# Kernel optimization log

Measured on AMD Instinct MI355X. Metric: run time of the kernel, lower is better.

The kernel has to match this reference:

```python
import jax, jax.numpy as jnp
import numpy as np

V, E, H, N, T, L = 32000, 1024, 1024, 64, 32, 196


def setup_inputs() -> dict:
    key = jax.random.key(0)
    ks = jax.random.split(key, 12)
    s = 0.02
    return {
        "inputs": jax.random.randint(ks[0], (N, T), 0, V, dtype=jnp.int32),
        "img_features": jax.random.normal(ks[1], (N, L, H), dtype=jnp.float32),
        "emb": jax.random.normal(ks[2], (V, E), dtype=jnp.float32) * s,
        "w_ih1": jax.random.normal(ks[3], (4 * H, E), dtype=jnp.float32) * s,
        "w_hh1": jax.random.normal(ks[4], (4 * H, H), dtype=jnp.float32) * s,
        "b_ih1": jax.random.normal(ks[5], (4 * H,), dtype=jnp.float32) * s,
        "b_hh1": jax.random.normal(ks[6], (4 * H,), dtype=jnp.float32) * s,
        "w_ih2": jax.random.normal(ks[7], (4 * H, 2 * H), dtype=jnp.float32) * s,
        "w_hh2": jax.random.normal(ks[8], (4 * H, H), dtype=jnp.float32) * s,
        "b_ih2": jax.random.normal(ks[9], (4 * H,), dtype=jnp.float32) * s,
        "b_hh2": jax.random.normal(ks[10], (4 * H,), dtype=jnp.float32) * s,
    }


def _lstm_cell(x, h, c, w_ih, w_hh, b_ih, b_hh):
    # PyTorch LSTMCell: gates ordered i, f, g, o
    g = x @ w_ih.T + b_ih + h @ w_hh.T + b_hh
    i, f, gg, o = jnp.split(g, 4, axis=-1)
    c_new = jax.nn.sigmoid(f) * c + jax.nn.sigmoid(i) * jnp.tanh(gg)
    h_new = jax.nn.sigmoid(o) * jnp.tanh(c_new)
    return h_new, c_new


def reference(inputs, img_features, emb, w_ih1, w_hh1, b_ih1, b_hh1,
              w_ih2, w_hh2, b_ih2, b_hh2):
    n, t = inputs.shape
    hdim = w_hh1.shape[1]
    embedded = emb[inputs]                      # (N, T, E)
    # faithful to original: .view(T, N, -1) is a reshape, NOT a transpose
    xs = embedded.reshape(t, n, -1)             # (T, N, E)

    def step(carry, x_t):
        h1, c1, h2, c2 = carry
        h1, c1 = _lstm_cell(x_t, h1, c1, w_ih1, w_hh1, b_ih1, b_hh1)
        # attention: raw dot-product weights (no softmax in original)
        alpha = jnp.einsum('nd,nld->nl', h1, img_features)   # (N, L)
        v_att = jnp.einsum('nl,nld->nd', alpha, img_features) # (N, D)
        x2 = jnp.concatenate([v_att, h1], axis=1)             # (N, 2H)
        h2, c2 = _lstm_cell(x2, h2, c2, w_ih2, w_hh2, b_ih2, b_hh2)
        return (h1, c1, h2, c2), h2

    zeros = jnp.zeros((n, hdim), dtype=img_features.dtype)
    init = (zeros, zeros, zeros, zeros)
    _, hs = jax.lax.scan(step, init, xs)        # (T, N, H)
    # faithful to original: cat along dim 0 then .view(N, T, -1) == reshape
    return hs.reshape(n, t, -1)
```

## Files before the change

kernel.cpp:

```cpp
#include <hip/hip_runtime.h>
#include <math.h>

typedef __attribute__((ext_vector_type(8))) short bf16x8;
typedef __attribute__((ext_vector_type(4))) short short4v;
typedef __attribute__((ext_vector_type(4))) float f32x4;

__device__ __forceinline__ float sigm(float x) { return 1.f / (1.f + expf(-x)); }

__device__ __forceinline__ float bf2f(short x) {
    unsigned u = ((unsigned)(unsigned short)x) << 16;
    float f; __builtin_memcpy(&f, &u, 4); return f;
}
__device__ __forceinline__ short f2bf(float f) {
    unsigned u; __builtin_memcpy(&u, &f, 4);
    unsigned r = (u + 0x7fffu + ((u >> 16) & 1u)) >> 16;
    return (short)r;
}

#define OFF_C1      0u
#define OFF_C2      262144u
#define OFF_H2A     524288u
#define OFF_H2B     655360u
#define OFF_H1HI    786432u
#define OFF_H1LO    5111808u
#define OFF_H1F     9437184u
#define OFF_X0HI    17825792u
#define OFF_X0LO    22020096u
#define OFF_B1      26214400u
#define OFF_B2      26230784u
#define OFF_WHH1HI  26247168u
#define OFF_WHH1LO  34635776u
#define OFF_WIH1HI  43024384u
#define OFF_WIH1LO  51412992u
#define OFF_WHH2HI  59801600u
#define OFF_WVHI    68190208u
#define OFF_WVLO    76578816u
#define OFF_WH2HI   84967424u
#define OFF_X12     93356032u

__global__ __launch_bounds__(256) void zero_ws(float4* __restrict__ p) {
    int i = blockIdx.x * 256 + threadIdx.x;
    p[i] = make_float4(0.f, 0.f, 0.f, 0.f);
}

__global__ __launch_bounds__(256) void perm_w_split(const float* __restrict__ src,
                                                    short* __restrict__ hi,
                                                    short* __restrict__ lo,
                                                    int rs, int co) {
    int idx = blockIdx.x * 256 + threadIdx.x;
    int jp = idx >> 8;
    int kq = idx & 255;
    int jsrc = (jp & 3) * 1024 + (jp >> 2);
    float4 v = *(const float4*)(src + (size_t)jsrc * rs + co + kq * 4);
    float a[4] = {v.x, v.y, v.z, v.w};
    short4v h, l;
    #pragma unroll
    for (int e = 0; e < 4; e++) {
        short q = f2bf(a[e]);
        h[e] = q;
        l[e] = f2bf(a[e] - bf2f(q));
    }
    *(short4v*)(hi + (size_t)jp * 1024 + kq * 4) = h;
    *(short4v*)(lo + (size_t)jp * 1024 + kq * 4) = l;
}

__global__ __launch_bounds__(256) void bias_prep(
    const float* __restrict__ bi1, const float* __restrict__ bh1,
    const float* __restrict__ bi2, const float* __restrict__ bh2,
    float* __restrict__ b1p, float* __restrict__ b2p) {
    int jp = blockIdx.x * 256 + threadIdx.x;
    int j = (jp & 3) * 1024 + (jp >> 2);
    b1p[jp] = bi1[j] + bh1[j];
    b2p[jp] = bi2[j] + bh2[j];
}

__global__ __launch_bounds__(256) void gather_x0_split(
    const int* __restrict__ tokens, const float* __restrict__ emb,
    short* __restrict__ hi, short* __restrict__ lo) {
    int idx = blockIdx.x * 256 + threadIdx.x;
    int p = idx >> 8;
    int k0 = (idx & 255) * 4;
    int tok = tokens[p];
    float4 v = *(const float4*)(emb + (size_t)tok * 1024 + k0);
    float a[4] = {v.x, v.y, v.z, v.w};
    short4v h, l;
    #pragma unroll
    for (int e = 0; e < 4; e++) {
        short q = f2bf(a[e]);
        h[e] = q;
        l[e] = f2bf(a[e] - bf2f(q));
    }
    *(short4v*)(hi + (size_t)p * 1024 + k0) = h;
    *(short4v*)(lo + (size_t)p * 1024 + k0) = l;
}

__global__ __launch_bounds__(256) void big_gemm(
    const short* __restrict__ A0, const short* __restrict__ A1s,
    const short* __restrict__ A2s, const short* __restrict__ A3s,
    const short* __restrict__ B0, const short* __restrict__ B1s,
    const short* __restrict__ B2s, const short* __restrict__ B3s,
    const float* __restrict__ bias, float* __restrict__ C, int K) {
    __shared__ short As[128 * 40];
    __shared__ short Bs[128 * 40];
    int tid = threadIdx.x;
    int n0 = blockIdx.x * 128;
    int m0 = blockIdx.y * 128;
    int lane = tid & 63, w = tid >> 6;
    int wm = (w >> 1) * 64, wn = (w & 1) * 64;
    int quad = lane >> 4, l16 = lane & 15;
    int srow = tid >> 2;
    int skc = (tid & 3) * 8;

    f32x4 acc[4][4];
    f32x4 z4 = {0.f, 0.f, 0.f, 0.f};
    #pragma unroll
    for (int i = 0; i < 4; i++)
        #pragma unroll
        for (int j = 0; j < 4; j++) acc[i][j] = z4;

    for (int k0 = 0; k0 < K; k0 += 32) {
        int seg = k0 >> 10;
        const short* Ab = (seg == 0) ? A0 : (seg == 1) ? A1s : (seg == 2) ? A2s : A3s;
        const short* Bb = (seg == 0) ? B0 : (seg == 1) ? B1s : (seg == 2) ? B2s : B3s;
        int kk = (k0 & 1023) + skc;
        const short* ga = Ab + (size_t)(m0 + srow) * 1024 + kk;
        const short* gb = Bb + (size_t)(n0 + srow) * 1024 + kk;
        bf16x8 av0 = *(const bf16x8*)ga;
        bf16x8 av1 = *(const bf16x8*)(ga + 64 * 1024);
        bf16x8 bv0 = *(const bf16x8*)gb;
        bf16x8 bv1 = *(const bf16x8*)(gb + 64 * 1024);
        __syncthreads();
        *(bf16x8*)&As[srow * 40 + skc] = av0;
        *(bf16x8*)&As[(srow + 64) * 40 + skc] = av1;
        *(bf16x8*)&Bs[srow * 40 + skc] = bv0;
        *(bf16x8*)&Bs[(srow + 64) * 40 + skc] = bv1;
        __syncthreads();
        bf16x8 af[4], bfr[4];
        #pragma unroll
        for (int im = 0; im < 4; im++)
            af[im] = *(const bf16x8*)&As[(wm + im * 16 + l16) * 40 + quad * 8];
        #pragma unroll
        for (int in = 0; in < 4; in++)
            bfr[in] = *(const bf16x8*)&Bs[(wn + in * 16 + l16) * 40 + quad * 8];
        #pragma unroll
        for (int im = 0; im < 4; im++)
            #pragma unroll
            for (int in = 0; in < 4; in++)
                acc[im][in] = __builtin_amdgcn_mfma_f32_16x16x32_bf16(
                    af[im], bfr[in], acc[im][in], 0, 0, 0);
    }
    #pragma unroll
    for (int in = 0; in < 4; in++) {
        int j = n0 + wn + in * 16 + l16;
        float bsv = bias[j];
        #pragma unroll
        for (int im = 0; im < 4; im++) {
            #pragma unroll
            for (int r = 0; r < 4; r++) {
                int p = m0 + wm + im * 16 + quad * 4 + r;
                C[(size_t)p * 4096 + j] = acc[im][in][r] + bsv;
            }
        }
    }
}

__global__ __launch_bounds__(256) void cell_step1(
    const short* __restrict__ Ahi, const short* __restrict__ Alo,
    const short* __restrict__ Whi, const short* __restrict__ Wlo,
    const float* __restrict__ Xg, float* __restrict__ c,
    short* __restrict__ hhi_o, short* __restrict__ hlo_o,
    float* __restrict__ hf_o) {
    __shared__ float red[4 * 64 * 16];
    int tid = threadIdx.x;
    int lane = tid & 63, w = tid >> 6;
    int quad = lane >> 4, l16 = lane & 15;
    int g = blockIdx.x;
    int kbase = w * 256;

    f32x4 acc[4];
    f32x4 z4 = {0.f, 0.f, 0.f, 0.f};
    acc[0] = z4; acc[1] = z4; acc[2] = z4; acc[3] = z4;

    const short* bh = Whi + (size_t)(g * 16 + l16) * 1024 + kbase + quad * 8;
    const short* bl = Wlo + (size_t)(g * 16 + l16) * 1024 + kbase + quad * 8;
    const short* ah = Ahi + (size_t)l16 * 1024 + kbase + quad * 8;
    const short* al = Alo + (size_t)l16 * 1024 + kbase + quad * 8;
    #pragma unroll
    for (int i = 0; i < 8; i++) {
        int k = i * 32;
        bf16x8 Bh = *(const bf16x8*)(bh + k);
        bf16x8 Bl = *(const bf16x8*)(bl + k);
        #pragma unroll
        for (int mt = 0; mt < 4; mt++) {
            bf16x8 Ah = *(const bf16x8*)(ah + mt * 16 * 1024 + k);
            bf16x8 Al = *(const bf16x8*)(al + mt * 16 * 1024 + k);
            acc[mt] = __builtin_amdgcn_mfma_f32_16x16x32_bf16(Ah, Bh, acc[mt], 0, 0, 0);
            acc[mt] = __builtin_amdgcn_mfma_f32_16x16x32_bf16(Al, Bh, acc[mt], 0, 0, 0);
            acc[mt] = __builtin_amdgcn_mfma_f32_16x16x32_bf16(Ah, Bl, acc[mt], 0, 0, 0);
        }
    }
    #pragma unroll
    for (int mt = 0; mt < 4; mt++)
        #pragma unroll
        for (int r = 0; r < 4; r++) {
            int s = mt * 16 + quad * 4 + r;
            red[(w * 64 + s) * 16 + l16] = acc[mt][r];
        }
    __syncthreads();

    int s = tid >> 2, dl = tid & 3;
    float gi = 0.f, gf = 0.f, gg = 0.f, go = 0.f;
    #pragma unroll
    for (int w2 = 0; w2 < 4; w2++) {
        const float* rp = &red[(w2 * 64 + s) * 16 + dl * 4];
        gi += rp[0]; gf += rp[1]; gg += rp[2]; go += rp[3];
    }
    float4 xg = *(const float4*)(Xg + (size_t)s * 4096 + g * 16 + dl * 4);
    gi += xg.x; gf += xg.y; gg += xg.z; go += xg.w;
    int d = g * 4 + dl;
    float cold = c[s * 1024 + d];
    float cn = sigm(gf) * cold + sigm(gi) * tanhf(gg);
    c[s * 1024 + d] = cn;
    float hn = sigm(go) * tanhf(cn);
    short q = f2bf(hn);
    hhi_o[s * 1024 + d] = q;
    hlo_o[s * 1024 + d] = f2bf(hn - bf2f(q));
    hf_o[s * 1024 + d] = hn;
}

__global__ __launch_bounds__(256) void cell_step2(
    const short* __restrict__ Aprev, const short* __restrict__ W,
    const float* __restrict__ Xg, float* __restrict__ c,
    short* __restrict__ hout_bf, float* __restrict__ hout_f32) {
    __shared__ float red[4 * 64 * 16];
    int tid = threadIdx.x;
    int lane = tid & 63, w = tid >> 6;
    int quad = lane >> 4, l16 = lane & 15;
    int g = blockIdx.x;
    int kbase = w * 256;

    f32x4 acc[4];
    f32x4 z4 = {0.f, 0.f, 0.f, 0.f};
    acc[0] = z4; acc[1] = z4; acc[2] = z4; acc[3] = z4;

    const short* brow = W + (size_t)(g * 16 + l16) * 1024 + kbase + quad * 8;
    const short* arow = Aprev + (size_t)l16 * 1024 + kbase + quad * 8;
    #pragma unroll
    for (int i = 0; i < 8; i++) {
        int k = i * 32;
        bf16x8 b = *(const bf16x8*)(brow + k);
        #pragma unroll
        for (int mt = 0; mt < 4; mt++) {
            bf16x8 a = *(const bf16x8*)(arow + mt * 16 * 1024 + k);
            acc[mt] = __builtin_amdgcn_mfma_f32_16x16x32_bf16(a, b, acc[mt], 0, 0, 0);
        }
    }
    #pragma unroll
    for (int mt = 0; mt < 4; mt++)
        #pragma unroll
        for (int r = 0; r < 4; r++) {
            int s = mt * 16 + quad * 4 + r;
            red[(w * 64 + s) * 16 + l16] = acc[mt][r];
        }
    __syncthreads();

    int s = tid >> 2, dl = tid & 3;
    float gi = 0.f, gf = 0.f, gg = 0.f, go = 0.f;
    #pragma unroll
    for (int w2 = 0; w2 < 4; w2++) {
        const float* rp = &red[(w2 * 64 + s) * 16 + dl * 4];
        gi += rp[0]; gf += rp[1]; gg += rp[2]; go += rp[3];
    }
    float4 xg = *(const float4*)(Xg + (size_t)s * 4096 + g * 16 + dl * 4);
    gi += xg.x; gf += xg.y; gg += xg.z; go += xg.w;
    int d = g * 4 + dl;
    float cold = c[s * 1024 + d];
    float cn = sigm(gf) * cold + sigm(gi) * tanhf(gg);
    c[s * 1024 + d] = cn;
    float hn = sigm(go) * tanhf(cn);
    hout_bf[s * 1024 + d] = f2bf(hn);
    hout_f32[s * 1024 + d] = hn;
}

__global__ __launch_bounds__(256) void attn_batch(
    const float* __restrict__ H1f, const float* __restrict__ F,
    short* __restrict__ Vhi, short* __restrict__ Vlo) {
    __shared__ float vs[4][4][1024];
    int n = blockIdx.x, tg = blockIdx.y;
    int tid = threadIdx.x, lane = tid & 63, w = tid >> 6;

    float h[4][16];
    #pragma unroll
    for (int tt = 0; tt < 4; tt++) {
        const float* hp = H1f + ((size_t)((tg * 4 + tt) * 64 + n)) * 1024 + lane * 16;
        #pragma unroll
        for (int j = 0; j < 4; j++) {
            float4 v = *(const float4*)(hp + j * 4);
            h[tt][j * 4 + 0] = v.x; h[tt][j * 4 + 1] = v.y;
            h[tt][j * 4 + 2] = v.z; h[tt][j * 4 + 3] = v.w;
        }
    }
    float vacc[4][16];
    #pragma unroll
    for (int tt = 0; tt < 4; tt++)
        #pragma unroll
        for (int j = 0; j < 16; j++) vacc[tt][j] = 0.f;

    const float* Fn = F + ((size_t)n * 196) * 1024 + lane * 16;
    for (int l = w; l < 196; l += 4) {
        const float* fr = Fn + (size_t)l * 1024;
        float f[16];
        #pragma unroll
        for (int j = 0; j < 4; j++) {
            float4 v = *(const float4*)(fr + j * 4);
            f[j * 4 + 0] = v.x; f[j * 4 + 1] = v.y;
            f[j * 4 + 2] = v.z; f[j * 4 + 3] = v.w;
        }
        float p[4] = {0.f, 0.f, 0.f, 0.f};
        #pragma unroll
        for (int tt = 0; tt < 4; tt++)
            #pragma unroll
            for (int j = 0; j < 16; j++) p[tt] += f[j] * h[tt][j];
        #pragma unroll
        for (int off = 32; off > 0; off >>= 1) {
            #pragma unroll
            for (int tt = 0; tt < 4; tt++) p[tt] += __shfl_xor(p[tt], off, 64);
        }
        #pragma unroll
        for (int tt = 0; tt < 4; tt++)
            #pragma unroll
            for (int j = 0; j < 16; j++) vacc[tt][j] += p[tt] * f[j];
    }
    #pragma unroll
    for (int tt = 0; tt < 4; tt++)
        #pragma unroll
        for (int j4 = 0; j4 < 4; j4++) {
            float4 v;
            v.x = vacc[tt][j4 * 4 + 0]; v.y = vacc[tt][j4 * 4 + 1];
            v.z = vacc[tt][j4 * 4 + 2]; v.w = vacc[tt][j4 * 4 + 3];
            *(float4*)&vs[w][tt][lane * 16 + j4 * 4] = v;
        }
    __syncthreads();
    int d0 = tid * 4;
    #pragma unroll
    for (int tt = 0; tt < 4; tt++) {
        float4 a = *(const float4*)&vs[0][tt][d0];
        float4 b = *(const float4*)&vs[1][tt][d0];
        float4 cc = *(const float4*)&vs[2][tt][d0];
        float4 e = *(const float4*)&vs[3][tt][d0];
        float sv[4];
        sv[0] = a.x + b.x + cc.x + e.x;
        sv[1] = a.y + b.y + cc.y + e.y;
        sv[2] = a.z + b.z + cc.z + e.z;
        sv[3] = a.w + b.w + cc.w + e.w;
        short4v b1, b2;
        #pragma unroll
        for (int e2 = 0; e2 < 4; e2++) {
            short q = f2bf(sv[e2]);
            b1[e2] = q;
            b2[e2] = f2bf(sv[e2] - bf2f(q));
        }
        size_t row = ((size_t)(tg * 4 + tt) * 64 + n) * 1024 + d0;
        *(short4v*)(Vhi + row) = b1;
        *(short4v*)(Vlo + row) = b2;
    }
}

extern "C" void kernel_launch(void* const* d_in, const int* in_sizes, int n_in,
                              void* d_out, int out_size, void* d_ws, size_t ws_size,
                              hipStream_t stream) {
    const int*   tokens = (const int*)d_in[0];
    const float* imgf   = (const float*)d_in[1];
    const float* emb    = (const float*)d_in[2];
    const float* w_ih1  = (const float*)d_in[3];
    const float* w_hh1  = (const float*)d_in[4];
    const float* b_ih1  = (const float*)d_in[5];
    const float* b_hh1  = (const float*)d_in[6];
    const float* w_ih2  = (const float*)d_in[7];
    const float* w_hh2  = (const float*)d_in[8];
    const float* b_ih2  = (const float*)d_in[9];
    const float* b_hh2  = (const float*)d_in[10];
    float* out = (float*)d_out;
    char* ws = (char*)d_ws;

    float* c1     = (float*)(ws + OFF_C1);
    float* c2     = (float*)(ws + OFF_C2);
    short* h2a    = (short*)(ws + OFF_H2A);
    short* h2b    = (short*)(ws + OFF_H2B);
    short* H1hi   = (short*)(ws + OFF_H1HI);
    short* H1lo   = (short*)(ws + OFF_H1LO);
    float* H1f    = (float*)(ws + OFF_H1F);
    short* X0hi   = (short*)(ws + OFF_X0HI);
    short* X0lo   = (short*)(ws + OFF_X0LO);
    short* Vhi    = (short*)(ws + OFF_X0HI);
    short* Vlo    = (short*)(ws + OFF_X0LO);
    float* bias1p = (float*)(ws + OFF_B1);
    float* bias2p = (float*)(ws + OFF_B2);
    short* whh1hi = (short*)(ws + OFF_WHH1HI);
    short* whh1lo = (short*)(ws + OFF_WHH1LO);
    short* wih1hi = (short*)(ws + OFF_WIH1HI);
    short* wih1lo = (short*)(ws + OFF_WIH1LO);
    short* whh2hi = (short*)(ws + OFF_WHH2HI);
    short* wvhi   = (short*)(ws + OFF_WVHI);
    short* wvlo   = (short*)(ws + OFF_WVLO);
    short* wh2hi  = (short*)(ws + OFF_WH2HI);
    float* X12    = (float*)(ws + OFF_X12);
    short* dump   = (short*)(ws + OFF_X12);

    zero_ws<<<192, 256, 0, stream>>>((float4*)(ws + OFF_C1));
    zero_ws<<<32, 256, 0, stream>>>((float4*)(ws + OFF_H1HI));
    zero_ws<<<32, 256, 0, stream>>>((float4*)(ws + OFF_H1LO));
    perm_w_split<<<4096, 256, 0, stream>>>(w_hh1, whh1hi, whh1lo, 1024, 0);
    perm_w_split<<<4096, 256, 0, stream>>>(w_ih1, wih1hi, wih1lo, 1024, 0);
    perm_w_split<<<4096, 256, 0, stream>>>(w_hh2, whh2hi, dump, 1024, 0);
    perm_w_split<<<4096, 256, 0, stream>>>(w_ih2, wvhi, wvlo, 2048, 0);
    perm_w_split<<<4096, 256, 0, stream>>>(w_ih2, wh2hi, dump, 2048, 1024);
    bias_prep<<<16, 256, 0, stream>>>(b_ih1, b_hh1, b_ih2, b_hh2, bias1p, bias2p);
    gather_x0_split<<<2048, 256, 0, stream>>>(tokens, emb, X0hi, X0lo);

    big_gemm<<<dim3(32, 16), 256, 0, stream>>>(
        X0hi, X0lo, X0hi, X0hi,
        wih1hi, wih1hi, wih1lo, wih1hi,
        bias1p, X12, 3072);

    for (int t = 0; t < 32; t++) {
        cell_step1<<<256, 256, 0, stream>>>(
            H1hi + (size_t)t * 65536, H1lo + (size_t)t * 65536,
            whh1hi, whh1lo, X12 + (size_t)t * 262144, c1,
            H1hi + (size_t)(t + 1) * 65536, H1lo + (size_t)(t + 1) * 65536,
            H1f + (size_t)t * 65536);
    }

    attn_batch<<<dim3(64, 8), 256, 0, stream>>>(H1f, imgf, Vhi, Vlo);

    big_gemm<<<dim3(32, 16), 256, 0, stream>>>(
        Vhi, Vlo, Vhi, H1hi + 65536,
        wvhi, wvhi, wvlo, wh2hi,
        bias2p, X12, 4096);

    for (int t = 0; t < 32; t++) {
        short* h2p = (t & 1) ? h2b : h2a;
        short* h2c = (t & 1) ? h2a : h2b;
        cell_step2<<<256, 256, 0, stream>>>(
            h2p, whh2hi, X12 + (size_t)t * 262144, c2,
            h2c, out + (size_t)t * 65536);
    }
}
```

Baseline: 1.189 ms.

## Replace per-timestep LSTM cell launches with persistent cooperative kernels using grid sync

The two recurrent loops, each 32 separate kernel launches, become one cooperative persistent kernel per layer. Each block holds its slice of the recurrent weights in registers for all timesteps and keeps the cell state in a register instead of global memory. Timesteps are separated by grid.sync(). This removes launch overhead, repeated weight reloads and the c-state round trips, at the cost of grid-barrier latency and higher register pressure.

```diff
diff --git a/kernel.cpp b/kernel.cpp
--- a/kernel.cpp
+++ b/kernel.cpp
@@ -1,5 +1,8 @@
 #include <hip/hip_runtime.h>
+#include <hip/hip_cooperative_groups.h>
 #include <math.h>
+
+namespace cg = cooperative_groups;
 
 typedef __attribute__((ext_vector_type(8))) short bf16x8;
 typedef __attribute__((ext_vector_type(4))) short short4v;
@@ -20,7 +23,6 @@
 #define OFF_C1      0u
 #define OFF_C2      262144u
 #define OFF_H2A     524288u
-#define OFF_H2B     655360u
 #define OFF_H1HI    786432u
 #define OFF_H1LO    5111808u
 #define OFF_H1F     9437184u
@@ -164,122 +166,134 @@
     }
 }
 
-__global__ __launch_bounds__(256) void cell_step1(
-    const short* __restrict__ Ahi, const short* __restrict__ Alo,
+__global__ __launch_bounds__(256) void pcell1(
     const short* __restrict__ Whi, const short* __restrict__ Wlo,
-    const float* __restrict__ Xg, float* __restrict__ c,
-    short* __restrict__ hhi_o, short* __restrict__ hlo_o,
-    float* __restrict__ hf_o) {
-    __shared__ float red[4 * 64 * 16];
+    const float* __restrict__ Xg, short* __restrict__ Hhi,
+    short* __restrict__ Hlo, float* __restrict__ Hf) {
+    __shared__ float red[4096];
+    cg::grid_group grid = cg::this_grid();
     int tid = threadIdx.x;
     int lane = tid & 63, w = tid >> 6;
     int quad = lane >> 4, l16 = lane & 15;
-    int g = blockIdx.x;
+    int b = blockIdx.x;
     int kbase = w * 256;
 
-    f32x4 acc[4];
-    f32x4 z4 = {0.f, 0.f, 0.f, 0.f};
-    acc[0] = z4; acc[1] = z4; acc[2] = z4; acc[3] = z4;
-
-    const short* bh = Whi + (size_t)(g * 16 + l16) * 1024 + kbase + quad * 8;
-    const short* bl = Wlo + (size_t)(g * 16 + l16) * 1024 + kbase + quad * 8;
-    const short* ah = Ahi + (size_t)l16 * 1024 + kbase + quad * 8;
-    const short* al = Alo + (size_t)l16 * 1024 + kbase + quad * 8;
-    #pragma unroll
-    for (int i = 0; i < 8; i++) {
-        int k = i * 32;
-        bf16x8 Bh = *(const bf16x8*)(bh + k);
-        bf16x8 Bl = *(const bf16x8*)(bl + k);
-        #pragma unroll
-        for (int mt = 0; mt < 4; mt++) {
-            bf16x8 Ah = *(const bf16x8*)(ah + mt * 16 * 1024 + k);
-            bf16x8 Al = *(const bf16x8*)(al + mt * 16 * 1024 + k);
-            acc[mt] = __builtin_amdgcn_mfma_f32_16x16x32_bf16(Ah, Bh, acc[mt], 0, 0, 0);
-            acc[mt] = __builtin_amdgcn_mfma_f32_16x16x32_bf16(Al, Bh, acc[mt], 0, 0, 0);
-            acc[mt] = __builtin_amdgcn_mfma_f32_16x16x32_bf16(Ah, Bl, acc[mt], 0, 0, 0);
-        }
-    }
-    #pragma unroll
-    for (int mt = 0; mt < 4; mt++)
-        #pragma unroll
-        for (int r = 0; r < 4; r++) {
-            int s = mt * 16 + quad * 4 + r;
-            red[(w * 64 + s) * 16 + l16] = acc[mt][r];
-        }
-    __syncthreads();
-
-    int s = tid >> 2, dl = tid & 3;
-    float gi = 0.f, gf = 0.f, gg = 0.f, go = 0.f;
-    #pragma unroll
-    for (int w2 = 0; w2 < 4; w2++) {
-        const float* rp = &red[(w2 * 64 + s) * 16 + dl * 4];
-        gi += rp[0]; gf += rp[1]; gg += rp[2]; go += rp[3];
-    }
-    float4 xg = *(const float4*)(Xg + (size_t)s * 4096 + g * 16 + dl * 4);
-    gi += xg.x; gf += xg.y; gg += xg.z; go += xg.w;
-    int d = g * 4 + dl;
-    float cold = c[s * 1024 + d];
-    float cn = sigm(gf) * cold + sigm(gi) * tanhf(gg);
-    c[s * 1024 + d] = cn;
-    float hn = sigm(go) * tanhf(cn);
-    short q = f2bf(hn);
-    hhi_o[s * 1024 + d] = q;
-    hlo_o[s * 1024 + d] = f2bf(hn - bf2f(q));
-    hf_o[s * 1024 + d] = hn;
-}
-
-__global__ __launch_bounds__(256) void cell_step2(
-    const short* __restrict__ Aprev, const short* __restrict__ W,
-    const float* __restrict__ Xg, float* __restrict__ c,
-    short* __restrict__ hout_bf, float* __restrict__ hout_f32) {
-    __shared__ float red[4 * 64 * 16];
+    bf16x8 whi[8], wlo[8];
+    {
+        const short* wp = Whi + (size_t)(b * 16 + l16) * 1024 + kbase + quad * 8;
+        const short* lp = Wlo + (size_t)(b * 16 + l16) * 1024 + kbase + quad * 8;
+        #pragma unroll
+        for (int i = 0; i < 8; i++) {
+            whi[i] = *(const bf16x8*)(wp + i * 32);
+            wlo[i] = *(const bf16x8*)(lp + i * 32);
+        }
+    }
+    int s_e = tid >> 2, dl = tid & 3;
+    int d = b * 4 + dl;
+    float c_reg = 0.f;
+
+    for (int t = 0; t < 32; t++) {
+        const short* ah = Hhi + (size_t)t * 65536 + (size_t)l16 * 1024 + kbase + quad * 8;
+        const short* al = Hlo + (size_t)t * 65536 + (size_t)l16 * 1024 + kbase + quad * 8;
+        f32x4 acc[4];
+        f32x4 z4 = {0.f, 0.f, 0.f, 0.f};
+        acc[0] = z4; acc[1] = z4; acc[2] = z4; acc[3] = z4;
+        #pragma unroll
+        for (int i = 0; i < 8; i++) {
+            int k = i * 32;
+            #pragma unroll
+            for (int mt = 0; mt < 4; mt++) {
+                bf16x8 Ah = *(const bf16x8*)(ah + mt * 16384 + k);
+                bf16x8 Al = *(const bf16x8*)(al + mt * 16384 + k);
+                acc[mt] = __builtin_amdgcn_mfma_f32_16x16x32_bf16(Ah, whi[i], acc[mt], 0, 0, 0);
+                acc[mt] = __builtin_amdgcn_mfma_f32_16x16x32_bf16(Al, whi[i], acc[mt], 0, 0, 0);
+                acc[mt] = __builtin_amdgcn_mfma_f32_16x16x32_bf16(Ah, wlo[i], acc[mt], 0, 0, 0);
+            }
+        }
+        __syncthreads();
+        #pragma unroll
+        for (int mt = 0; mt < 4; mt++)
+            #pragma unroll
+            for (int r = 0; r < 4; r++)
+                red[(w * 64 + mt * 16 + quad * 4 + r) * 16 + l16] = acc[mt][r];
+        __syncthreads();
+        float gi = 0.f, gf = 0.f, gg = 0.f, go = 0.f;
+        #pragma unroll
+        for (int w2 = 0; w2 < 4; w2++) {
+            const float* rp = &red[(w2 * 64 + s_e) * 16 + dl * 4];
+            gi += rp[0]; gf += rp[1]; gg += rp[2]; go += rp[3];
+        }
+        float4 xg = *(const float4*)(Xg + (size_t)(t * 64 + s_e) * 4096 + b * 16 + dl * 4);
+        gi += xg.x; gf += xg.y; gg += xg.z; go += xg.w;
+        float cn = sigm(gf) * c_reg + sigm(gi) * tanhf(gg);
+        c_reg = cn;
+        float hn = sigm(go) * tanhf(cn);
+        short q = f2bf(hn);
+        size_t o = (size_t)(t + 1) * 65536 + (size_t)s_e * 1024 + d;
+        Hhi[o] = q;
+        Hlo[o] = f2bf(hn - bf2f(q));
+        Hf[(size_t)t * 65536 + (size_t)s_e * 1024 + d] = hn;
+        grid.sync();
+    }
+}
+
+__global__ __launch_bounds__(256) void pcell2(
+    const short* __restrict__ Whi, const float* __restrict__ Xg,
+    short* __restrict__ H2, float* __restrict__ out) {
+    __shared__ float red[4096];
+    cg::grid_group grid = cg::this_grid();
     int tid = threadIdx.x;
     int lane = tid & 63, w = tid >> 6;
     int quad = lane >> 4, l16 = lane & 15;
-    int g = blockIdx.x;
+    int b = blockIdx.x;
     int kbase = w * 256;
 
-    f32x4 acc[4];
-    f32x4 z4 = {0.f, 0.f, 0.f, 0.f};
-    acc[0] = z4; acc[1] = z4; acc[2] = z4; acc[3] = z4;
-
-    const short* brow = W + (size_t)(g * 16 + l16) * 1024 + kbase + quad * 8;
-    const short* arow = Aprev + (size_t)l16 * 1024 + kbase + quad * 8;
-    #pragma unroll
-    for (int i = 0; i < 8; i++) {
-        int k = i * 32;
-        bf16x8 b = *(const bf16x8*)(brow + k);
-        #pragma unroll
-        for (int mt = 0; mt < 4; mt++) {
-            bf16x8 a = *(const bf16x8*)(arow + mt * 16 * 1024 + k);
-            acc[mt] = __builtin_amdgcn_mfma_f32_16x16x32_bf16(a, b, acc[mt], 0, 0, 0);
-        }
-    }
-    #pragma unroll
-    for (int mt = 0; mt < 4; mt++)
-        #pragma unroll
-        for (int r = 0; r < 4; r++) {
-            int s = mt * 16 + quad * 4 + r;
-            red[(w * 64 + s) * 16 + l16] = acc[mt][r];
-        }
-    __syncthreads();
-
-    int s = tid >> 2, dl = tid & 3;
-    float gi = 0.f, gf = 0.f, gg = 0.f, go = 0.f;
-    #pragma unroll
-    for (int w2 = 0; w2 < 4; w2++) {
-        const float* rp = &red[(w2 * 64 + s) * 16 + dl * 4];
-        gi += rp[0]; gf += rp[1]; gg += rp[2]; go += rp[3];
-    }
-    float4 xg = *(const float4*)(Xg + (size_t)s * 4096 + g * 16 + dl * 4);
-    gi += xg.x; gf += xg.y; gg += xg.z; go += xg.w;
-    int d = g * 4 + dl;
-    float cold = c[s * 1024 + d];
-    float cn = sigm(gf) * cold + sigm(gi) * tanhf(gg);
-    c[s * 1024 + d] = cn;
-    float hn = sigm(go) * tanhf(cn);
-    hout_bf[s * 1024 + d] = f2bf(hn);
-    hout_f32[s * 1024 + d] = hn;
+    bf16x8 whi[8];
+    {
+        const short* wp = Whi + (size_t)(b * 16 + l16) * 1024 + kbase + quad * 8;
+        #pragma unroll
+        for (int i = 0; i < 8; i++) whi[i] = *(const bf16x8*)(wp + i * 32);
+    }
+    int s_e = tid >> 2, dl = tid & 3;
+    int d = b * 4 + dl;
+    float c_reg = 0.f;
+
+    for (int t = 0; t < 32; t++) {
+        const short* ah = H2 + (size_t)(t & 1) * 65536 + (size_t)l16 * 1024 + kbase + quad * 8;
+        f32x4 acc[4];
+        f32x4 z4 = {0.f, 0.f, 0.f, 0.f};
+        acc[0] = z4; acc[1] = z4; acc[2] = z4; acc[3] = z4;
+        #pragma unroll
+        for (int i = 0; i < 8; i++) {
+            int k = i * 32;
+            #pragma unroll
+            for (int mt = 0; mt < 4; mt++) {
+                bf16x8 Ah = *(const bf16x8*)(ah + mt * 16384 + k);
+                acc[mt] = __builtin_amdgcn_mfma_f32_16x16x32_bf16(Ah, whi[i], acc[mt], 0, 0, 0);
+            }
+        }
+        __syncthreads();
+        #pragma unroll
+        for (int mt = 0; mt < 4; mt++)
+            #pragma unroll
+            for (int r = 0; r < 4; r++)
+                red[(w * 64 + mt * 16 + quad * 4 + r) * 16 + l16] = acc[mt][r];
+        __syncthreads();
+        float gi = 0.f, gf = 0.f, gg = 0.f, go = 0.f;
+        #pragma unroll
+        for (int w2 = 0; w2 < 4; w2++) {
+            const float* rp = &red[(w2 * 64 + s_e) * 16 + dl * 4];
+            gi += rp[0]; gf += rp[1]; gg += rp[2]; go += rp[3];
+        }
+        float4 xg = *(const float4*)(Xg + (size_t)(t * 64 + s_e) * 4096 + b * 16 + dl * 4);
+        gi += xg.x; gf += xg.y; gg += xg.z; go += xg.w;
+        float cn = sigm(gf) * c_reg + sigm(gi) * tanhf(gg);
+        c_reg = cn;
+        float hn = sigm(go) * tanhf(cn);
+        H2[(size_t)((t + 1) & 1) * 65536 + (size_t)s_e * 1024 + d] = f2bf(hn);
+        out[(size_t)t * 65536 + (size_t)s_e * 1024 + d] = hn;
+        grid.sync();
+    }
 }
 
 __global__ __launch_bounds__(256) void attn_batch(
@@ -383,10 +397,7 @@
     float* out = (float*)d_out;
     char* ws = (char*)d_ws;
 
-    float* c1     = (float*)(ws + OFF_C1);
-    float* c2     = (float*)(ws + OFF_C2);
-    short* h2a    = (short*)(ws + OFF_H2A);
-    short* h2b    = (short*)(ws + OFF_H2B);
+    short* H2     = (short*)(ws + OFF_H2A);
     short* H1hi   = (short*)(ws + OFF_H1HI);
     short* H1lo   = (short*)(ws + OFF_H1LO);
     float* H1f    = (float*)(ws + OFF_H1F);
@@ -407,7 +418,7 @@
     float* X12    = (float*)(ws + OFF_X12);
     short* dump   = (short*)(ws + OFF_X12);
 
-    zero_ws<<<192, 256, 0, stream>>>((float4*)(ws + OFF_C1));
+    zero_ws<<<64, 256, 0, stream>>>((float4*)(ws + OFF_H2A));
     zero_ws<<<32, 256, 0, stream>>>((float4*)(ws + OFF_H1HI));
     zero_ws<<<32, 256, 0, stream>>>((float4*)(ws + OFF_H1LO));
     perm_w_split<<<4096, 256, 0, stream>>>(w_hh1, whh1hi, whh1lo, 1024, 0);
@@ -423,12 +434,13 @@
         wih1hi, wih1hi, wih1lo, wih1hi,
         bias1p, X12, 3072);
 
-    for (int t = 0; t < 32; t++) {
-        cell_step1<<<256, 256, 0, stream>>>(
-            H1hi + (size_t)t * 65536, H1lo + (size_t)t * 65536,
-            whh1hi, whh1lo, X12 + (size_t)t * 262144, c1,
-            H1hi + (size_t)(t + 1) * 65536, H1lo + (size_t)(t + 1) * 65536,
-            H1f + (size_t)t * 65536);
+    {
+        const short* a_whi = whh1hi;
+        const short* a_wlo = whh1lo;
+        const float* a_xg  = X12;
+        void* args[] = {(void*)&a_whi, (void*)&a_wlo, (void*)&a_xg,
+                        (void*)&H1hi, (void*)&H1lo, (void*)&H1f};
+        hipLaunchCooperativeKernel((void*)pcell1, dim3(256), dim3(256), args, 0, stream);
     }
 
     attn_batch<<<dim3(64, 8), 256, 0, stream>>>(H1f, imgf, Vhi, Vlo);
@@ -438,11 +450,10 @@
         wvhi, wvhi, wvlo, wh2hi,
         bias2p, X12, 4096);
 
-    for (int t = 0; t < 32; t++) {
-        short* h2p = (t & 1) ? h2b : h2a;
-        short* h2c = (t & 1) ? h2a : h2b;
-        cell_step2<<<256, 256, 0, stream>>>(
-            h2p, whh2hi, X12 + (size_t)t * 262144, c2,
-            h2c, out + (size_t)t * 65536);
-    }
-}
+    {
+        const short* a_w  = whh2hi;
+        const float* a_xg = X12;
+        void* args[] = {(void*)&a_w, (void*)&a_xg, (void*)&H2, (void*)&out};
+        hipLaunchCooperativeKernel((void*)pcell2, dim3(256), dim3(256), args, 0, stream);
+    }
+}
```

Measured after the change: 3.167 ms. 166% more time.
